# Kernel tuning notes

Measured on AMD Instinct MI355X. Metric: run time of the kernel, lower is better.

Reference implementation:

```python
import jax, jax.numpy as jnp
import numpy as np

B, S, V, D, H, L = 2, 1024, 32000, 1024, 16, 4
DK = D // H
DF = 4 * D
EPS = 1e-5


def setup_inputs() -> dict:
    key = jax.random.key(0)
    ks = jax.random.split(key, 9)
    s = 0.02
    rn = lambda k, shape: jax.random.normal(k, shape, jnp.float32) * s
    return {
        "input_ids": jax.random.randint(ks[0], (B, S), 0, V, dtype=jnp.int32),
        "emb": rn(ks[1], (V, D)),
        "Wq": rn(ks[2], (L, D, D)),
        "Wk": rn(ks[3], (L, D, D)),
        "Wv": rn(ks[4], (L, D, D)),
        "Wo": rn(ks[5], (L, D, D)),
        "W1": rn(ks[6], (L, D, DF)),
        "b1": jnp.zeros((L, DF), jnp.float32),
        "W2": rn(ks[7], (L, DF, D)),
        "b2": jnp.zeros((L, D), jnp.float32),
        "ln1_g": jnp.ones((L, D), jnp.float32),
        "ln1_b": jnp.zeros((L, D), jnp.float32),
        "ln2_g": jnp.ones((L, D), jnp.float32),
        "ln2_b": jnp.zeros((L, D), jnp.float32),
        "lnf_g": jnp.ones((D,), jnp.float32),
        "lnf_b": jnp.zeros((D,), jnp.float32),
        "head_w": rn(ks[8], (D, V)),
    }


def _ln(x, g, b):
    m = jnp.mean(x, -1, keepdims=True)
    v = jnp.mean(jnp.square(x - m), -1, keepdims=True)
    return (x - m) * jax.lax.rsqrt(v + EPS) * g + b


def _heads(x):
    # [B,S,D] -> [B,H,S,DK]
    return x.reshape(B, S, H, DK).transpose(0, 2, 1, 3)


def _forward(input_ids, emb, Wq, Wk, Wv, Wo, W1, b1, W2, b2,
             ln1_g, ln1_b, ln2_g, ln2_b, lnf_g, lnf_b, head_w):
    x = emb[input_ids]  # [B,S,D]
    # causal mask: position q attends to k <= q (prefill, no past)
    mask = jnp.triu(jnp.full((S, S), -jnp.inf, jnp.float32), k=1)
    scale = 1.0 / np.sqrt(DK).astype(np.float32)

    def block(x, p):
        wq, wk, wv, wo, w1, bb1, w2, bb2, g1, be1, g2, be2 = p
        h = _ln(x, g1, be1)
        q = _heads(h @ wq)
        k = _heads(h @ wk)
        v = _heads(h @ wv)
        scores = jnp.einsum('bhqd,bhkd->bhqk', q, k) * scale + mask
        a = jax.nn.softmax(scores, axis=-1)
        o = jnp.einsum('bhqk,bhkd->bhqd', a, v)
        o = o.transpose(0, 2, 1, 3).reshape(B, S, D) @ wo
        x = x + o
        h2 = _ln(x, g2, be2)
        x = x + jax.nn.gelu(h2 @ w1 + bb1, approximate=False) @ w2 + bb2
        return x, None

    x, _ = jax.lax.scan(block, x, (Wq, Wk, Wv, Wo, W1, b1, W2, b2,
                                   ln1_g, ln1_b, ln2_g, ln2_b))
    logits = _ln(x, lnf_g, lnf_b) @ head_w  # [B,S,V]
    return logits


def reference(input_ids, emb, Wq, Wk, Wv, Wo, W1, b1, W2, b2,
              ln1_g, ln1_b, ln2_g, ln2_b, lnf_g, lnf_b, head_w):
    return _forward(input_ids, emb, Wq, Wk, Wv, Wo, W1, b1, W2, b2,
                    ln1_g, ln1_b, ln2_g, ln2_b, lnf_g, lnf_b, head_w)
```

## Files before the change

### kernel.cpp

```cpp
#include <hip/hip_runtime.h>
#include <stdint.h>

#define B_ 2
#define S_ 1024
#define V_ 32000
#define D_ 1024
#define H_ 16
#define L_ 4
#define DF_ 4096
#define M_ (B_*S_)

typedef short short8 __attribute__((ext_vector_type(8)));
typedef float f32x4 __attribute__((ext_vector_type(4)));

__device__ __forceinline__ unsigned short f2bf(float f){
  union { float f; unsigned int u; } v; v.f = f;
  unsigned int u = v.u;
  u = u + 0x7fffu + ((u >> 16) & 1u);
  return (unsigned short)(u >> 16);
}

__device__ __forceinline__ void gload16(const void* g, void* l){
  __builtin_amdgcn_global_load_lds(
      (__attribute__((address_space(1))) void*)(uintptr_t)g,
      (__attribute__((address_space(3))) void*)(uintptr_t)l, 16, 0, 0);
}

__global__ __launch_bounds__(256) void embed_k(const int* __restrict__ ids,
    const float* __restrict__ emb, float* __restrict__ x){
  int row = blockIdx.x;
  int id = ids[row];
  float4 v = reinterpret_cast<const float4*>(emb + (size_t)id*D_)[threadIdx.x];
  reinterpret_cast<float4*>(x + (size_t)row*D_)[threadIdx.x] = v;
}

__global__ __launch_bounds__(256) void ln_k(const float* __restrict__ x,
    const float* __restrict__ g, const float* __restrict__ b,
    unsigned short* __restrict__ out){
  int row = blockIdx.x;
  int tid = threadIdx.x;
  float4 v = reinterpret_cast<const float4*>(x + (size_t)row*D_)[tid];
  float s = v.x+v.y+v.z+v.w;
  float ss = v.x*v.x + v.y*v.y + v.z*v.z + v.w*v.w;
  #pragma unroll
  for (int off=1; off<64; off<<=1){ s += __shfl_xor(s, off); ss += __shfl_xor(ss, off); }
  __shared__ float rs[4], rss[4];
  int wave = tid>>6, lane = tid&63;
  if (lane==0){ rs[wave]=s; rss[wave]=ss; }
  __syncthreads();
  s  = rs[0]+rs[1]+rs[2]+rs[3];
  ss = rss[0]+rss[1]+rss[2]+rss[3];
  float mean = s * (1.0f/(float)D_);
  float var  = ss * (1.0f/(float)D_) - mean*mean;
  float inv = rsqrtf(var + 1e-5f);
  float4 gg = reinterpret_cast<const float4*>(g)[tid];
  float4 bb = reinterpret_cast<const float4*>(b)[tid];
  ushort4 o;
  o.x = f2bf((v.x-mean)*inv*gg.x + bb.x);
  o.y = f2bf((v.y-mean)*inv*gg.y + bb.y);
  o.z = f2bf((v.z-mean)*inv*gg.z + bb.z);
  o.w = f2bf((v.w-mean)*inv*gg.w + bb.w);
  reinterpret_cast<ushort4*>(out + (size_t)row*D_)[tid] = o;
}

__global__ __launch_bounds__(256) void transpose_k(const float* __restrict__ in,
    unsigned short* __restrict__ out, int K, int N, size_t in_ls, size_t out_ls){
  __shared__ float t[64][65];
  const float* inp = in + (size_t)blockIdx.z*in_ls;
  unsigned short* outp = out + (size_t)blockIdx.z*out_ls;
  int k0 = blockIdx.y*64, n0 = blockIdx.x*64;
  int rr = threadIdx.x >> 4, c4 = (threadIdx.x & 15)*4;
  #pragma unroll
  for (int i=0;i<4;i++){
    float4 v = *reinterpret_cast<const float4*>(inp + (size_t)(k0+rr+i*16)*N + n0 + c4);
    t[rr+i*16][c4+0]=v.x; t[rr+i*16][c4+1]=v.y; t[rr+i*16][c4+2]=v.z; t[rr+i*16][c4+3]=v.w;
  }
  __syncthreads();
  #pragma unroll
  for (int i=0;i<4;i++){
    int n = rr + i*16;
    ushort4 o;
    o.x = f2bf(t[c4+0][n]); o.y = f2bf(t[c4+1][n]);
    o.z = f2bf(t[c4+2][n]); o.w = f2bf(t[c4+3][n]);
    *reinterpret_cast<ushort4*>(outp + (size_t)(n0+n)*K + k0 + c4) = o;
  }
}

template<int EP>
__global__ __launch_bounds__(256)
void gemm_bt(const unsigned short* __restrict__ A, const unsigned short* __restrict__ B,
             void* __restrict__ C, const float* __restrict__ bias,
             const float* __restrict__ resid, int K, int ldc, int MB, int kLen){
  __shared__ unsigned short As[2][128*64];
  __shared__ unsigned short Bs[2][128*64];
  const int tid = threadIdx.x;
  const int wave = tid>>6, lane = tid&63;
  const int wm = wave>>1, wn = wave&1;
  const int nwg = gridDim.x;
  const int p = blockIdx.x;
  const int t = (nwg & 7) ? p : ((p & 7)*(nwg>>3) + (p>>3));
  const int by = t % MB, bx = t / MB;
  const int row0 = by*128, col0 = bx*128;
  const int kz = blockIdx.z;
  const int k0 = kz*kLen;
  f32x4 acc[4][4] = {};
  const int sw8 = ((lane&7) ^ ((lane>>3)&7))*8;
  const unsigned short* Ag = A + (size_t)(row0 + wave*8 + (lane>>3))*K + sw8;
  const unsigned short* Bg = B + (size_t)(col0 + wave*8 + (lane>>3))*K + sw8;
  const int r = lane&15, g16 = lane>>4;
  const int rsw = (r&7)<<4;
#define STAGE_BT(buf, kt) do{ \
    _Pragma("unroll") \
    for (int i=0;i<4;i++){ \
      gload16(Ag + (size_t)i*32*K + (kt), As[buf] + (wave*8 + i*32)*64); \
      gload16(Bg + (size_t)i*32*K + (kt), Bs[buf] + (wave*8 + i*32)*64); \
    } }while(0)
  STAGE_BT(0, k0);
  __syncthreads();
  int cur = 0;
  for (int kt=k0; kt<k0+kLen; kt+=64){
    if (kt + 64 < k0 + kLen) STAGE_BT(cur^1, kt+64);
    #pragma unroll
    for (int ks=0; ks<2; ks++){
      short8 a[4], b[4];
      #pragma unroll
      for (int m=0;m<4;m++)
        a[m] = *reinterpret_cast<const short8*>((const char*)As[cur] + (wm*64+m*16+r)*128 + ((ks*64 + g16*16) ^ rsw));
      #pragma unroll
      for (int n=0;n<4;n++)
        b[n] = *reinterpret_cast<const short8*>((const char*)Bs[cur] + (wn*64+n*16+r)*128 + ((ks*64 + g16*16) ^ rsw));
      #pragma unroll
      for (int m=0;m<4;m++)
        #pragma unroll
        for (int n=0;n<4;n++)
          acc[m][n] = __builtin_amdgcn_mfma_f32_16x16x32_bf16(a[m], b[n], acc[m][n], 0,0,0);
    }
    __syncthreads();
    cur ^= 1;
  }
  float* Cp5 = (float*)C + (size_t)kz*M_*ldc;
  #pragma unroll
  for (int m=0;m<4;m++){
    const int row = row0 + wm*64 + m*16 + g16*4;
    #pragma unroll
    for (int n=0;n<4;n++){
      const int col = col0 + wn*64 + n*16 + r;
      #pragma unroll
      for (int j=0;j<4;j++){
        float val = acc[m][n][j];
        size_t idx = (size_t)(row+j)*ldc + col;
        if constexpr (EP==2 || EP==3) val += bias[col];
        if constexpr (EP==2) val = 0.5f*val*(1.0f + erff(val*0.70710678118f));
        if constexpr (EP==1 || EP==3) val += resid[idx];
        if constexpr (EP==0 || EP==2) ((unsigned short*)C)[idx] = f2bf(val);
        else if constexpr (EP==5) Cp5[idx] = val;
        else ((float*)C)[idx] = val;
      }
    }
  }
}

#define LDA8(buf,m,ks) (*(const short8*)(lds8 + (buf)*65536 + (wm*128+(m)*16+r)*128 + (((ks)*64+g16*16)^rsw)))
#define LDB8(buf,n,ks) (*(const short8*)(lds8 + (buf)*65536 + 32768 + (wn*64+(n)*16+r)*128 + (((ks)*64+g16*16)^rsw)))
#define STG(buf,isB,h,i,tile) gload16( \
    ((isB) ? Bw + (size_t)(col0 + (h)*128 + (i)*64 + wave*8 + srow)*K + (size_t)(tile)*64 + scsw \
           : A  + (size_t)(row0 + (h)*128 + (i)*64 + wave*8 + srow)*K + (size_t)(tile)*64 + scsw), \
    lds8 + (buf)*65536 + (isB)*32768 + ((h)*128 + (i)*64 + wave*8)*128 )
#define STG_HT(buf,isB,h,tile) do{ STG(buf,isB,h,0,tile); STG(buf,isB,h,1,tile); }while(0)
#define BLOAD8(bT) do{ \
  bfr[0][0]=LDB8(bT,0,0); bfr[0][1]=LDB8(bT,0,1); bfr[1][0]=LDB8(bT,1,0); bfr[1][1]=LDB8(bT,1,1); \
  bfr[2][0]=LDB8(bT,2,0); bfr[2][1]=LDB8(bT,2,1); bfr[3][0]=LDB8(bT,3,0); bfr[3][1]=LDB8(bT,3,1); }while(0)
#define MM8(mb,n) do{ \
  acc[mb][n]    =__builtin_amdgcn_mfma_f32_16x16x32_bf16(a0[0],bfr[n][0],acc[mb][n],0,0,0); \
  acc[mb][n]    =__builtin_amdgcn_mfma_f32_16x16x32_bf16(a0[1],bfr[n][1],acc[mb][n],0,0,0); \
  acc[(mb)+1][n]=__builtin_amdgcn_mfma_f32_16x16x32_bf16(a1[0],bfr[n][0],acc[(mb)+1][n],0,0,0); \
  acc[(mb)+1][n]=__builtin_amdgcn_mfma_f32_16x16x32_bf16(a1[1],bfr[n][1],acc[(mb)+1][n],0,0,0); }while(0)
#define VMC(n)  asm volatile("s_waitcnt vmcnt(" #n ")" ::: "memory")
#define PH8(bT, mb, STAGES, TAIL) do{ \
  short8 a0[2], a1[2]; \
  a0[0]=LDA8(bT,mb,0); a0[1]=LDA8(bT,mb,1); a1[0]=LDA8(bT,(mb)+1,0); a1[1]=LDA8(bT,(mb)+1,1); \
  STAGES; \
  __builtin_amdgcn_s_barrier(); \
  asm volatile("s_waitcnt lgkmcnt(0)" ::: "memory"); \
  __builtin_amdgcn_sched_barrier(0); \
  __builtin_amdgcn_s_setprio(1); \
  MM8(mb,0); MM8(mb,1); MM8(mb,2); MM8(mb,3); \
  __builtin_amdgcn_s_setprio(0); \
  TAIL; \
  __builtin_amdgcn_s_barrier(); \
  __builtin_amdgcn_sched_barrier(0); \
}while(0)

__global__ __launch_bounds__(512, 2)
void gemm_8ph(const unsigned short* __restrict__ A, const unsigned short* __restrict__ Bw,
              float* __restrict__ C, int K, int ldc, int MB){
  __shared__ char lds8[131072];
  const int tid = threadIdx.x;
  const int wave = tid>>6, lane = tid&63;
  const int wm = wave>>2, wn = wave&3;
  const int nwg = gridDim.x;
  const int pp = blockIdx.x;
  const int t = (nwg & 7) ? pp : ((pp & 7)*(nwg>>3) + (pp>>3));
  const int by = t % MB, bx = t / MB;
  const int row0 = by*256, col0 = bx*256;
  const int r = lane&15, g16 = lane>>4;
  const int rsw = (r&7)<<4;
  const int srow = lane>>3;
  const int scsw = ((lane&7) ^ srow)*8;

  f32x4 acc[8][4] = {};
  short8 bfr[4][2];
  const int NT = K/64;

  STG_HT(0,1,0,0); STG_HT(0,1,1,0);
  STG_HT(0,0,0,0); STG_HT(0,0,1,0);
  STG_HT(1,1,0,1); STG_HT(1,1,1,1);
  VMC(4);
  __builtin_amdgcn_s_barrier();
  __builtin_amdgcn_sched_barrier(0);

  for (int T0 = 0; T0 < NT; T0 += 2){
    const bool last = (T0 + 2 >= NT);
    BLOAD8(0);
    PH8(0, 0, { STG_HT(1,0,0,T0+1); STG_HT(1,0,1,T0+1); }, ((void)0));
    PH8(0, 2, { if(!last) STG_HT(0,1,0,T0+2); }, ((void)0));
    if (last) PH8(0, 4, ((void)0), VMC(0));
    else      PH8(0, 4, STG_HT(0,1,1,T0+2), VMC(4));
    PH8(0, 6, ((void)0), ((void)0));
    BLOAD8(1);
    PH8(1, 0, { if(!last){ STG_HT(0,0,0,T0+2); STG_HT(0,0,1,T0+2); } }, ((void)0));
    PH8(1, 2, { if(!last) STG_HT(1,1,0,T0+3); }, ((void)0));
    if (last) PH8(1, 4, ((void)0), ((void)0));
    else      PH8(1, 4, STG_HT(1,1,1,T0+3), VMC(4));
    PH8(1, 6, ((void)0), ((void)0));
  }

  #pragma unroll
  for (int m=0;m<8;m++){
    const int row = row0 + wm*128 + m*16 + g16*4;
    #pragma unroll
    for (int n=0;n<4;n++){
      const int col = col0 + wn*64 + n*16 + r;
      #pragma unroll
      for (int j=0;j<4;j++)
        C[(size_t)(row+j)*ldc + col] = acc[m][n][j];
    }
  }
}

__global__ __launch_bounds__(256) void reduce_k(float* __restrict__ x,
    const float* __restrict__ part, const float* __restrict__ bias, int ldc, int KS){
  size_t idx = (size_t)blockIdx.x*256 + threadIdx.x;
  float4 v = reinterpret_cast<const float4*>(part)[idx];
  for (int z=1; z<KS; z++){
    float4 p = reinterpret_cast<const float4*>(part)[(size_t)z*((size_t)M_*ldc/4) + idx];
    v.x+=p.x; v.y+=p.y; v.z+=p.z; v.w+=p.w;
  }
  if (bias){
    float4 b = reinterpret_cast<const float4*>(bias)[idx % (size_t)(ldc/4)];
    v.x+=b.x; v.y+=b.y; v.z+=b.z; v.w+=b.w;
  }
  float4 xx = reinterpret_cast<float4*>(x)[idx];
  v.x+=xx.x; v.y+=xx.y; v.z+=xx.z; v.w+=xx.w;
  reinterpret_cast<float4*>(x)[idx] = v;
}

__global__ __launch_bounds__(256)
void attn_k(const unsigned short* __restrict__ qkv, unsigned short* __restrict__ o){
  __shared__ unsigned short Ks[64*64];
  __shared__ unsigned short Vt[64*64];
  __shared__ unsigned short Ps[4*16*64];
  const int tid = threadIdx.x;
  const int wave = tid>>6, lane = tid&63;
  const int qb = blockIdx.x, h = blockIdx.y, b = blockIdx.z;
  const int r = lane&15, g = lane>>4;
  const size_t rowbase = (size_t)b*S_*3*D_;
  short8 qf[2];
  {
    const unsigned short* qp = qkv + rowbase + (size_t)(qb*64 + wave*16 + r)*(3*D_) + h*64 + g*8;
    qf[0] = *reinterpret_cast<const short8*>(qp);
    qf[1] = *reinterpret_cast<const short8*>(qp + 32);
  }
  float mrow[4] = {-INFINITY,-INFINITY,-INFINITY,-INFINITY};
  float lrow[4] = {0.f,0.f,0.f,0.f};
  f32x4 oacc[4] = {};
  const int qglob0 = qb*64 + wave*16 + g*4;
  unsigned short* Pw = Ps + wave*16*64;

  for (int kt=0; kt<=qb; kt++){
    __syncthreads();
    #pragma unroll
    for (int i=0;i<2;i++){
      int key = i*32 + (tid>>3);
      int c8 = (tid&7)*8;
      const unsigned short* kp = qkv + rowbase + (size_t)(kt*64+key)*(3*D_) + D_ + h*64 + c8;
      uint4 kd = *reinterpret_cast<const uint4*>(kp);
      int bo = (key*128 + c8*2) ^ ((key&7)<<4);
      *reinterpret_cast<uint4*>((char*)Ks + bo) = kd;
      const unsigned short* vp = qkv + rowbase + (size_t)(kt*64+key)*(3*D_) + 2*D_ + h*64 + c8;
      uint4 vd = *reinterpret_cast<const uint4*>(vp);
      const unsigned short* ve = reinterpret_cast<const unsigned short*>(&vd);
      #pragma unroll
      for (int j=0;j<8;j++){
        int d = c8 + j;
        int bo2 = (d*128 + key*2) ^ ((d&7)<<4);
        *reinterpret_cast<unsigned short*>((char*)Vt + bo2) = ve[j];
      }
    }
    __syncthreads();
    f32x4 sacc[4] = {};
    #pragma unroll
    for (int ks=0; ks<2; ks++){
      #pragma unroll
      for (int nb=0; nb<4; nb++){
        int key = nb*16 + r;
        int bo = (key*128 + (ks*32+g*8)*2) ^ ((key&7)<<4);
        short8 kf = *reinterpret_cast<const short8*>((char*)Ks + bo);
        sacc[nb] = __builtin_amdgcn_mfma_f32_16x16x32_bf16(qf[ks], kf, sacc[nb], 0,0,0);
      }
    }
    float sv[4][4];
    float tm[4] = {-INFINITY,-INFINITY,-INFINITY,-INFINITY};
    #pragma unroll
    for (int nb=0; nb<4; nb++){
      int key = kt*64 + nb*16 + r;
      #pragma unroll
      for (int j=0;j<4;j++){
        float s = sacc[nb][j]*0.125f;
        s = (key <= qglob0 + j) ? s : -INFINITY;
        sv[nb][j] = s;
        tm[j] = fmaxf(tm[j], s);
      }
    }
    #pragma unroll
    for (int off=1; off<16; off<<=1){
      #pragma unroll
      for (int j=0;j<4;j++) tm[j] = fmaxf(tm[j], __shfl_xor(tm[j], off));
    }
    float sf[4], psum[4];
    #pragma unroll
    for (int j=0;j<4;j++){
      float mn = fmaxf(mrow[j], tm[j]);
      sf[j] = __expf(mrow[j]-mn);
      mrow[j] = mn;
      psum[j] = 0.0f;
    }
    #pragma unroll
    for (int nb=0; nb<4; nb++){
      #pragma unroll
      for (int j=0;j<4;j++){
        float p = __expf(sv[nb][j]-mrow[j]);
        psum[j] += p;
        int prow = g*4+j;
        int bo = (prow*128 + (nb*16+r)*2) ^ ((prow&7)<<4);
        *reinterpret_cast<unsigned short*>((char*)Pw + bo) = f2bf(p);
      }
    }
    #pragma unroll
    for (int off=1; off<16; off<<=1){
      #pragma unroll
      for (int j=0;j<4;j++) psum[j] += __shfl_xor(psum[j], off);
    }
    #pragma unroll
    for (int j=0;j<4;j++) lrow[j] = lrow[j]*sf[j] + psum[j];
    #pragma unroll
    for (int nb=0;nb<4;nb++){
      #pragma unroll
      for (int j=0;j<4;j++) oacc[nb][j] *= sf[j];
    }
    asm volatile("s_waitcnt lgkmcnt(0)" ::: "memory");
    #pragma unroll
    for (int ks=0; ks<2; ks++){
      int bo = (r*128 + (ks*32+g*8)*2) ^ ((r&7)<<4);
      short8 pf = *reinterpret_cast<const short8*>((char*)Pw + bo);
      #pragma unroll
      for (int nb=0; nb<4; nb++){
        int d = nb*16 + r;
        int bo2 = (d*128 + (ks*32+g*8)*2) ^ ((d&7)<<4);
        short8 vf = *reinterpret_cast<const short8*>((char*)Vt + bo2);
        oacc[nb] = __builtin_amdgcn_mfma_f32_16x16x32_bf16(pf, vf, oacc[nb], 0,0,0);
      }
    }
  }
  #pragma unroll
  for (int nb=0; nb<4; nb++){
    #pragma unroll
    for (int j=0;j<4;j++){
      float ov = oacc[nb][j] / lrow[j];
      size_t row = (size_t)b*S_ + qb*64 + wave*16 + g*4 + j;
      o[row*D_ + h*64 + nb*16 + r] = f2bf(ov);
    }
  }
}

extern "C" void kernel_launch(void* const* d_in, const int* in_sizes, int n_in,
                              void* d_out, int out_size, void* d_ws, size_t ws_size,
                              hipStream_t stream) {
  const int*   ids   = (const int*)  d_in[0];
  const float* emb   = (const float*)d_in[1];
  const float* Wq    = (const float*)d_in[2];
  const float* Wk    = (const float*)d_in[3];
  const float* Wv    = (const float*)d_in[4];
  const float* Wo    = (const float*)d_in[5];
  const float* W1    = (const float*)d_in[6];
  const float* b1    = (const float*)d_in[7];
  const float* W2    = (const float*)d_in[8];
  const float* b2    = (const float*)d_in[9];
  const float* ln1_g = (const float*)d_in[10];
  const float* ln1_b = (const float*)d_in[11];
  const float* ln2_g = (const float*)d_in[12];
  const float* ln2_b = (const float*)d_in[13];
  const float* lnf_g = (const float*)d_in[14];
  const float* lnf_b = (const float*)d_in[15];
  const float* headw = (const float*)d_in[16];

  unsigned short* ws = (unsigned short*)d_ws;
  unsigned short* wqkvT = ws;
  unsigned short* woT   = wqkvT + (size_t)L_*3*D_*D_;
  unsigned short* w1T   = woT   + (size_t)L_*D_*D_;
  unsigned short* w2T   = w1T   + (size_t)L_*D_*DF_;
  unsigned short* headT = w2T   + (size_t)L_*D_*DF_;
  unsigned short* h     = headT + (size_t)V_*D_;
  unsigned short* qkv   = h     + (size_t)M_*D_;
  unsigned short* attno = qkv   + (size_t)M_*3*D_;
  unsigned short* h2    = attno + (size_t)M_*D_;
  float*          x     = (float*)(h2 + (size_t)M_*DF_);
  float*          part  = x + (size_t)M_*D_;
  size_t needed = ((char*)(part + (size_t)4*M_*D_)) - (char*)d_ws;
  const bool splitk = (ws_size >= needed);

  transpose_k<<<dim3(D_/64, D_/64, L_), 256, 0, stream>>>(Wq, wqkvT,            D_, D_, (size_t)D_*D_, (size_t)3*D_*D_);
  transpose_k<<<dim3(D_/64, D_/64, L_), 256, 0, stream>>>(Wk, wqkvT + D_*D_,    D_, D_, (size_t)D_*D_, (size_t)3*D_*D_);
  transpose_k<<<dim3(D_/64, D_/64, L_), 256, 0, stream>>>(Wv, wqkvT + 2*D_*D_,  D_, D_, (size_t)D_*D_, (size_t)3*D_*D_);
  transpose_k<<<dim3(D_/64, D_/64, L_), 256, 0, stream>>>(Wo, woT,              D_, D_, (size_t)D_*D_, (size_t)D_*D_);
  transpose_k<<<dim3(DF_/64, D_/64, L_), 256, 0, stream>>>(W1, w1T,             D_, DF_, (size_t)D_*DF_, (size_t)D_*DF_);
  transpose_k<<<dim3(D_/64, DF_/64, L_), 256, 0, stream>>>(W2, w2T,             DF_, D_, (size_t)D_*DF_, (size_t)D_*DF_);
  transpose_k<<<dim3(V_/64, D_/64, 1), 256, 0, stream>>>(headw, headT,          D_, V_, 0, 0);

  embed_k<<<M_, 256, 0, stream>>>(ids, emb, x);

  for (int l = 0; l < L_; l++){
    ln_k<<<M_, 256, 0, stream>>>(x, ln1_g + l*D_, ln1_b + l*D_, h);
    gemm_bt<0><<<dim3((3*D_/128)*(M_/128), 1, 1), 256, 0, stream>>>(h, wqkvT + (size_t)l*3*D_*D_, qkv, nullptr, nullptr, D_, 3*D_, M_/128, D_);
    attn_k<<<dim3(S_/64, H_, B_), 256, 0, stream>>>(qkv, attno);
    if (splitk){
      gemm_bt<5><<<dim3((D_/128)*(M_/128), 1, 4), 256, 0, stream>>>(attno, woT + (size_t)l*D_*D_, part, nullptr, nullptr, D_, D_, M_/128, D_/4);
      reduce_k<<<(M_*D_/4)/256, 256, 0, stream>>>(x, part, nullptr, D_, 4);
    } else {
      gemm_bt<1><<<dim3((D_/128)*(M_/128), 1, 1), 256, 0, stream>>>(attno, woT + (size_t)l*D_*D_, x, nullptr, x, D_, D_, M_/128, D_);
    }
    ln_k<<<M_, 256, 0, stream>>>(x, ln2_g + l*D_, ln2_b + l*D_, h);
    gemm_bt<2><<<dim3((DF_/128)*(M_/128), 1, 1), 256, 0, stream>>>(h, w1T + (size_t)l*D_*DF_, h2, b1 + l*DF_, nullptr, D_, DF_, M_/128, D_);
    if (splitk){
      gemm_bt<5><<<dim3((D_/128)*(M_/128), 1, 4), 256, 0, stream>>>(h2, w2T + (size_t)l*D_*DF_, part, nullptr, nullptr, DF_, D_, M_/128, DF_/4);
      reduce_k<<<(M_*D_/4)/256, 256, 0, stream>>>(x, part, b2 + l*D_, D_, 4);
    } else {
      gemm_bt<3><<<dim3((D_/128)*(M_/128), 1, 1), 256, 0, stream>>>(h2, w2T + (size_t)l*D_*DF_, x, b2 + l*D_, x, DF_, D_, M_/128, DF_);
    }
  }

  ln_k<<<M_, 256, 0, stream>>>(x, lnf_g, lnf_b, h);
  gemm_8ph<<<dim3((V_/256)*(M_/256), 1, 1), 512, 0, stream>>>(h, headT, (float*)d_out, D_, V_, M_/256);
}
```

Baseline: 968.9 us.

## Fuse split-K reduction with LayerNorm, halve split-K, restructure LM-head GEMM loop

Replaces the separate split-K reduce kernel plus the following LayerNorm with one rln_k kernel. It sums the partials, bias and residual, writes x, and emits the normalized bf16 activation for the next GEMM, so x is not read back a second time. The next layer's LN1 and the final LN are folded into the FFN down-projection's reduction. Split-K drops from 4 to 2, which halves partial-buffer traffic but leaves fewer workgroups per GEMM. The LM-head GEMM loop peels its last iteration to remove the branches, spreads loads more evenly across phases, and drops the sched_barriers, which may change instruction scheduling.

```diff
diff --git a/kernel.cpp b/kernel.cpp
--- a/kernel.cpp
+++ b/kernel.cpp
@@ -40,6 +40,45 @@
   int row = blockIdx.x;
   int tid = threadIdx.x;
   float4 v = reinterpret_cast<const float4*>(x + (size_t)row*D_)[tid];
+  float s = v.x+v.y+v.z+v.w;
+  float ss = v.x*v.x + v.y*v.y + v.z*v.z + v.w*v.w;
+  #pragma unroll
+  for (int off=1; off<64; off<<=1){ s += __shfl_xor(s, off); ss += __shfl_xor(ss, off); }
+  __shared__ float rs[4], rss[4];
+  int wave = tid>>6, lane = tid&63;
+  if (lane==0){ rs[wave]=s; rss[wave]=ss; }
+  __syncthreads();
+  s  = rs[0]+rs[1]+rs[2]+rs[3];
+  ss = rss[0]+rss[1]+rss[2]+rss[3];
+  float mean = s * (1.0f/(float)D_);
+  float var  = ss * (1.0f/(float)D_) - mean*mean;
+  float inv = rsqrtf(var + 1e-5f);
+  float4 gg = reinterpret_cast<const float4*>(g)[tid];
+  float4 bb = reinterpret_cast<const float4*>(b)[tid];
+  ushort4 o;
+  o.x = f2bf((v.x-mean)*inv*gg.x + bb.x);
+  o.y = f2bf((v.y-mean)*inv*gg.y + bb.y);
+  o.z = f2bf((v.z-mean)*inv*gg.z + bb.z);
+  o.w = f2bf((v.w-mean)*inv*gg.w + bb.w);
+  reinterpret_cast<ushort4*>(out + (size_t)row*D_)[tid] = o;
+}
+
+__global__ __launch_bounds__(256) void rln_k(float* __restrict__ x,
+    const float* __restrict__ part, const float* __restrict__ bias,
+    const float* __restrict__ g, const float* __restrict__ b,
+    unsigned short* __restrict__ out, int KS){
+  int row = blockIdx.x;
+  int tid = threadIdx.x;
+  float4 v = reinterpret_cast<const float4*>(x + (size_t)row*D_)[tid];
+  for (int z=0; z<KS; z++){
+    float4 p = reinterpret_cast<const float4*>(part + (size_t)z*M_*D_ + (size_t)row*D_)[tid];
+    v.x+=p.x; v.y+=p.y; v.z+=p.z; v.w+=p.w;
+  }
+  if (bias){
+    float4 bb4 = reinterpret_cast<const float4*>(bias)[tid];
+    v.x+=bb4.x; v.y+=bb4.y; v.z+=bb4.z; v.w+=bb4.w;
+  }
+  reinterpret_cast<float4*>(x + (size_t)row*D_)[tid] = v;
   float s = v.x+v.y+v.z+v.w;
   float ss = v.x*v.x + v.y*v.y + v.z*v.z + v.w*v.w;
   #pragma unroll
@@ -182,13 +221,11 @@
   STAGES; \
   __builtin_amdgcn_s_barrier(); \
   asm volatile("s_waitcnt lgkmcnt(0)" ::: "memory"); \
-  __builtin_amdgcn_sched_barrier(0); \
   __builtin_amdgcn_s_setprio(1); \
   MM8(mb,0); MM8(mb,1); MM8(mb,2); MM8(mb,3); \
   __builtin_amdgcn_s_setprio(0); \
   TAIL; \
   __builtin_amdgcn_s_barrier(); \
-  __builtin_amdgcn_sched_barrier(0); \
 }while(0)
 
 __global__ __launch_bounds__(512, 2)
@@ -217,23 +254,29 @@
   STG_HT(1,1,0,1); STG_HT(1,1,1,1);
   VMC(4);
   __builtin_amdgcn_s_barrier();
-  __builtin_amdgcn_sched_barrier(0);
-
-  for (int T0 = 0; T0 < NT; T0 += 2){
-    const bool last = (T0 + 2 >= NT);
+
+  for (int T0 = 0; T0 < NT-2; T0 += 2){
     BLOAD8(0);
-    PH8(0, 0, { STG_HT(1,0,0,T0+1); STG_HT(1,0,1,T0+1); }, ((void)0));
-    PH8(0, 2, { if(!last) STG_HT(0,1,0,T0+2); }, ((void)0));
-    if (last) PH8(0, 4, ((void)0), VMC(0));
-    else      PH8(0, 4, STG_HT(0,1,1,T0+2), VMC(4));
-    PH8(0, 6, ((void)0), ((void)0));
+    PH8(0, 0, STG_HT(1,0,0,T0+1), ((void)0));
+    PH8(0, 2, STG_HT(1,0,1,T0+1), ((void)0));
+    PH8(0, 4, STG_HT(0,1,0,T0+2), ((void)0));
+    PH8(0, 6, STG_HT(0,1,1,T0+2), VMC(4));
     BLOAD8(1);
-    PH8(1, 0, { if(!last){ STG_HT(0,0,0,T0+2); STG_HT(0,0,1,T0+2); } }, ((void)0));
-    PH8(1, 2, { if(!last) STG_HT(1,1,0,T0+3); }, ((void)0));
-    if (last) PH8(1, 4, ((void)0), ((void)0));
-    else      PH8(1, 4, STG_HT(1,1,1,T0+3), VMC(4));
-    PH8(1, 6, ((void)0), ((void)0));
-  }
+    PH8(1, 0, STG_HT(0,0,0,T0+2), ((void)0));
+    PH8(1, 2, STG_HT(0,0,1,T0+2), ((void)0));
+    PH8(1, 4, STG_HT(1,1,0,T0+3), ((void)0));
+    PH8(1, 6, STG_HT(1,1,1,T0+3), VMC(4));
+  }
+  BLOAD8(0);
+  PH8(0, 0, STG_HT(1,0,0,NT-1), ((void)0));
+  PH8(0, 2, STG_HT(1,0,1,NT-1), ((void)0));
+  PH8(0, 4, ((void)0), ((void)0));
+  PH8(0, 6, ((void)0), VMC(0));
+  BLOAD8(1);
+  PH8(1, 0, ((void)0), ((void)0));
+  PH8(1, 2, ((void)0), ((void)0));
+  PH8(1, 4, ((void)0), ((void)0));
+  PH8(1, 6, ((void)0), ((void)0));
 
   #pragma unroll
   for (int m=0;m<8;m++){
@@ -246,23 +289,6 @@
         C[(size_t)(row+j)*ldc + col] = acc[m][n][j];
     }
   }
-}
-
-__global__ __launch_bounds__(256) void reduce_k(float* __restrict__ x,
-    const float* __restrict__ part, const float* __restrict__ bias, int ldc, int KS){
-  size_t idx = (size_t)blockIdx.x*256 + threadIdx.x;
-  float4 v = reinterpret_cast<const float4*>(part)[idx];
-  for (int z=1; z<KS; z++){
-    float4 p = reinterpret_cast<const float4*>(part)[(size_t)z*((size_t)M_*ldc/4) + idx];
-    v.x+=p.x; v.y+=p.y; v.z+=p.z; v.w+=p.w;
-  }
-  if (bias){
-    float4 b = reinterpret_cast<const float4*>(bias)[idx % (size_t)(ldc/4)];
-    v.x+=b.x; v.y+=b.y; v.z+=b.z; v.w+=b.w;
-  }
-  float4 xx = reinterpret_cast<float4*>(x)[idx];
-  v.x+=xx.x; v.y+=xx.y; v.z+=xx.z; v.w+=xx.w;
-  reinterpret_cast<float4*>(x)[idx] = v;
 }
 
 __global__ __launch_bounds__(256)
@@ -426,7 +452,7 @@
   unsigned short* h2    = attno + (size_t)M_*D_;
   float*          x     = (float*)(h2 + (size_t)M_*DF_);
   float*          part  = x + (size_t)M_*D_;
-  size_t needed = ((char*)(part + (size_t)4*M_*D_)) - (char*)d_ws;
+  size_t needed = ((char*)(part + (size_t)2*M_*D_)) - (char*)d_ws;
   const bool splitk = (ws_size >= needed);
 
   transpose_k<<<dim3(D_/64, D_/64, L_), 256, 0, stream>>>(Wq, wqkvT,            D_, D_, (size_t)D_*D_, (size_t)3*D_*D_);
@@ -438,27 +464,29 @@
   transpose_k<<<dim3(V_/64, D_/64, 1), 256, 0, stream>>>(headw, headT,          D_, V_, 0, 0);
 
   embed_k<<<M_, 256, 0, stream>>>(ids, emb, x);
+  ln_k<<<M_, 256, 0, stream>>>(x, ln1_g, ln1_b, h);
 
   for (int l = 0; l < L_; l++){
-    ln_k<<<M_, 256, 0, stream>>>(x, ln1_g + l*D_, ln1_b + l*D_, h);
     gemm_bt<0><<<dim3((3*D_/128)*(M_/128), 1, 1), 256, 0, stream>>>(h, wqkvT + (size_t)l*3*D_*D_, qkv, nullptr, nullptr, D_, 3*D_, M_/128, D_);
     attn_k<<<dim3(S_/64, H_, B_), 256, 0, stream>>>(qkv, attno);
     if (splitk){
-      gemm_bt<5><<<dim3((D_/128)*(M_/128), 1, 4), 256, 0, stream>>>(attno, woT + (size_t)l*D_*D_, part, nullptr, nullptr, D_, D_, M_/128, D_/4);
-      reduce_k<<<(M_*D_/4)/256, 256, 0, stream>>>(x, part, nullptr, D_, 4);
+      gemm_bt<5><<<dim3((D_/128)*(M_/128), 1, 2), 256, 0, stream>>>(attno, woT + (size_t)l*D_*D_, part, nullptr, nullptr, D_, D_, M_/128, D_/2);
+      rln_k<<<M_, 256, 0, stream>>>(x, part, nullptr, ln2_g + l*D_, ln2_b + l*D_, h, 2);
     } else {
       gemm_bt<1><<<dim3((D_/128)*(M_/128), 1, 1), 256, 0, stream>>>(attno, woT + (size_t)l*D_*D_, x, nullptr, x, D_, D_, M_/128, D_);
-    }
-    ln_k<<<M_, 256, 0, stream>>>(x, ln2_g + l*D_, ln2_b + l*D_, h);
+      ln_k<<<M_, 256, 0, stream>>>(x, ln2_g + l*D_, ln2_b + l*D_, h);
+    }
     gemm_bt<2><<<dim3((DF_/128)*(M_/128), 1, 1), 256, 0, stream>>>(h, w1T + (size_t)l*D_*DF_, h2, b1 + l*DF_, nullptr, D_, DF_, M_/128, D_);
+    const float* ng = (l+1 < L_) ? (ln1_g + (l+1)*D_) : lnf_g;
+    const float* nb = (l+1 < L_) ? (ln1_b + (l+1)*D_) : lnf_b;
     if (splitk){
-      gemm_bt<5><<<dim3((D_/128)*(M_/128), 1, 4), 256, 0, stream>>>(h2, w2T + (size_t)l*D_*DF_, part, nullptr, nullptr, DF_, D_, M_/128, DF_/4);
-      reduce_k<<<(M_*D_/4)/256, 256, 0, stream>>>(x, part, b2 + l*D_, D_, 4);
+      gemm_bt<5><<<dim3((D_/128)*(M_/128), 1, 2), 256, 0, stream>>>(h2, w2T + (size_t)l*D_*DF_, part, nullptr, nullptr, DF_, D_, M_/128, DF_/2);
+      rln_k<<<M_, 256, 0, stream>>>(x, part, b2 + l*D_, ng, nb, h, 2);
     } else {
       gemm_bt<3><<<dim3((D_/128)*(M_/128), 1, 1), 256, 0, stream>>>(h2, w2T + (size_t)l*D_*DF_, x, b2 + l*D_, x, DF_, D_, M_/128, DF_);
-    }
-  }
-
-  ln_k<<<M_, 256, 0, stream>>>(x, lnf_g, lnf_b, h);
+      ln_k<<<M_, 256, 0, stream>>>(x, ng, nb, h);
+    }
+  }
+
   gemm_8ph<<<dim3((V_/256)*(M_/256), 1, 1), 512, 0, stream>>>(h, headT, (float*)d_out, D_, V_, M_/256);
 }
```

Measured after the change: 952.9 us. No clear change (-1.6%).
